# Kernel tuning notes

Hardware: AMD Instinct MI355X
Metric: run time of the kernel (lower is better)

## Reference

```python
import jax, jax.numpy as jnp
import numpy as np

B, C, H, W = 4, 512, 64, 64
C8 = C // 8


def setup_inputs() -> dict:
    key = jax.random.key(0)
    ks = jax.random.split(key, 8)
    return {
        "x": jax.random.normal(ks[0], (B, C, H, W), jnp.float32),
        "wb": jax.random.normal(ks[1], (C8, C), jnp.float32) * 0.05,
        "bb": jax.random.normal(ks[2], (C8,), jnp.float32) * 0.05,
        "wc": jax.random.normal(ks[3], (C8, C), jnp.float32) * 0.05,
        "bc": jax.random.normal(ks[4], (C8,), jnp.float32) * 0.05,
        "wd": jax.random.normal(ks[5], (C, C), jnp.float32) * 0.05,
        "bd": jax.random.normal(ks[6], (C,), jnp.float32) * 0.05,
        "alpha": jax.random.normal(ks[7], (1,), jnp.float32),
    }


def reference(x, wb, bb, wc, bc, wd, bd, alpha):
    b, c, h, w = x.shape
    n = h * w
    xf = x.reshape(b, c, n)  # [B, C, N]
    # 1x1 convs == per-pixel channel matmuls
    feat_b = jnp.einsum('kc,bcn->bkn', wb, xf) + bb[:, None]  # [B, C/8, N]
    feat_c = jnp.einsum('kc,bcn->bkn', wc, xf) + bc[:, None]  # [B, C/8, N]
    # attention_s[n, m] = softmax_m( feat_b[:, n] . feat_c[:, m] )  (no scaling, as in source)
    scores = jnp.einsum('bkn,bkm->bnm', feat_b, feat_c)  # [B, N, N]
    attn = jax.nn.softmax(scores, axis=-1)
    feat_d = jnp.einsum('oc,bcn->bon', wd, xf) + bd[:, None]  # [B, C, N]
    # feat_e = bmm(feat_d, attn^T): fe[c, n] = sum_m fd[c, m] * attn[n, m]
    feat_e = jnp.einsum('bcm,bnm->bcn', feat_d, attn).reshape(b, c, h, w)
    return alpha[0] * feat_e + x
```

## Files before the change

### kernel.cpp

```cpp
#include <hip/hip_runtime.h>
#include <hip/hip_bf16.h>

#define NB 4
#define CC 512
#define CK 64
#define NN 4096

typedef unsigned short u16;
typedef __attribute__((ext_vector_type(8))) __bf16 bf16x8;
typedef __attribute__((ext_vector_type(4))) float f32x4;
typedef __attribute__((ext_vector_type(4))) unsigned int u32x4;
typedef __attribute__((ext_vector_type(8))) unsigned short u16x8;
typedef __attribute__((ext_vector_type(4))) unsigned short u16x4;

__device__ __forceinline__ u16 f2b(float f) {
  union { float f; unsigned u; } x; x.f = f;
  unsigned r = x.u + 0x7fffu + ((x.u >> 16) & 1u);
  return (u16)(r >> 16);
}
__device__ __forceinline__ float b2f(u16 u) {
  union { unsigned u; float f; } x; x.u = ((unsigned)u) << 16; return x.f;
}

#define MFMA16(a, b, c) __builtin_amdgcn_mfma_f32_16x16x32_bf16((a), (b), (c), 0, 0, 0)

__global__ __launch_bounds__(256) void proj_qk(
    const float* __restrict__ x,
    const float* __restrict__ wb, const float* __restrict__ bb,
    const float* __restrict__ wc, const float* __restrict__ bc,
    u16* __restrict__ Qhi, u16* __restrict__ Qlo,
    u16* __restrict__ Khi, u16* __restrict__ Klo)
{
  const int tid = threadIdx.x;
  const int n0 = blockIdx.x * 64;
  const int which = blockIdx.y;
  const int b = blockIdx.z;
  const float* w   = which ? wc : wb;
  const float* bia = which ? bc : bb;
  u16* oh = which ? Khi : Qhi;
  u16* ol = which ? Klo : Qlo;

  __shared__ u16 Wh[64][40], Wl[64][40], Xh[64][40], Xl[64][40];

  const int lane = tid & 63, wid = tid >> 6;
  const int wr = wid >> 1, wn = wid & 1;
  const int l15 = lane & 15, lk = (lane >> 4) * 8;

  f32x4 acc[2][2] = {};

  for (int kk = 0; kk < CC; kk += 32) {
    {
      const int row = tid >> 2, c0 = (tid & 3) * 8;
      const float* src = w + (size_t)row * CC + kk + c0;
#pragma unroll
      for (int i = 0; i < 8; ++i) {
        float v = src[i];
        u16 h = f2b(v);
        Wh[row][c0 + i] = h;
        Wl[row][c0 + i] = f2b(v - b2f(h));
      }
    }
    {
      const int cc2 = tid >> 3, j0 = (tid & 7) * 8;
      const float* src = x + ((size_t)b * CC + kk + cc2) * NN + n0 + j0;
#pragma unroll
      for (int i = 0; i < 8; ++i) {
        float v = src[i];
        u16 h = f2b(v);
        Xh[j0 + i][cc2] = h;
        Xl[j0 + i][cc2] = f2b(v - b2f(h));
      }
    }
    __syncthreads();
#pragma unroll
    for (int fi = 0; fi < 2; ++fi) {
      const int ar = wr * 32 + fi * 16 + l15;
      bf16x8 ah = *(const bf16x8*)&Wh[ar][lk];
      bf16x8 al = *(const bf16x8*)&Wl[ar][lk];
#pragma unroll
      for (int fj = 0; fj < 2; ++fj) {
        const int br = wn * 32 + fj * 16 + l15;
        bf16x8 bh = *(const bf16x8*)&Xh[br][lk];
        bf16x8 bl = *(const bf16x8*)&Xl[br][lk];
        acc[fi][fj] = MFMA16(ah, bh, acc[fi][fj]);
        acc[fi][fj] = MFMA16(ah, bl, acc[fi][fj]);
        acc[fi][fj] = MFMA16(al, bh, acc[fi][fj]);
      }
    }
    __syncthreads();
  }

#pragma unroll
  for (int fi = 0; fi < 2; ++fi) {
    const int d0 = wr * 32 + fi * 16 + (lane >> 4) * 4;
#pragma unroll
    for (int fj = 0; fj < 2; ++fj) {
      const int n = n0 + wn * 32 + fj * 16 + l15;
      u16x4 vh, vl;
#pragma unroll
      for (int r = 0; r < 4; ++r) {
        float v = acc[fi][fj][r] + bia[d0 + r];
        u16 h = f2b(v);
        vh[r] = h;
        vl[r] = f2b(v - b2f(h));
      }
      *(u16x4*)&oh[((size_t)b * NN + n) * CK + d0] = vh;
      *(u16x4*)&ol[((size_t)b * NN + n) * CK + d0] = vl;
    }
  }
}

__global__ __launch_bounds__(256) void proj_v(
    const float* __restrict__ x,
    const float* __restrict__ wd, const float* __restrict__ bd,
    u16* __restrict__ Vt)
{
  const int tid = threadIdx.x;
  const int n0 = blockIdx.x * 64;
  const int o0 = blockIdx.y * 64;
  const int b = blockIdx.z;

  __shared__ u16 Wt[64][40], Xt[64][40];
  const int lane = tid & 63, wid = tid >> 6;
  const int wr = wid >> 1, wn = wid & 1;
  const int l15 = lane & 15, lk = (lane >> 4) * 8;

  f32x4 acc[2][2] = {};
  for (int kk = 0; kk < CC; kk += 32) {
    {
      const int row = tid >> 2, c0 = (tid & 3) * 8;
      const float* src = wd + (size_t)(o0 + row) * CC + kk + c0;
#pragma unroll
      for (int i = 0; i < 8; ++i) Wt[row][c0 + i] = f2b(src[i]);
    }
    {
      const int cc2 = tid >> 3, j0 = (tid & 7) * 8;
      const float* src = x + ((size_t)b * CC + kk + cc2) * NN + n0 + j0;
#pragma unroll
      for (int i = 0; i < 8; ++i) Xt[j0 + i][cc2] = f2b(src[i]);
    }
    __syncthreads();
#pragma unroll
    for (int fi = 0; fi < 2; ++fi) {
      bf16x8 a = *(const bf16x8*)&Wt[wr * 32 + fi * 16 + l15][lk];
#pragma unroll
      for (int fj = 0; fj < 2; ++fj) {
        bf16x8 bv = *(const bf16x8*)&Xt[wn * 32 + fj * 16 + l15][lk];
        acc[fi][fj] = MFMA16(a, bv, acc[fi][fj]);
      }
    }
    __syncthreads();
  }
#pragma unroll
  for (int fi = 0; fi < 2; ++fi) {
    const int d0 = o0 + wr * 32 + fi * 16 + (lane >> 4) * 4;
#pragma unroll
    for (int fj = 0; fj < 2; ++fj) {
      const int n = n0 + wn * 32 + fj * 16 + l15;
#pragma unroll
      for (int r = 0; r < 4; ++r)
        Vt[((size_t)b * CC + d0 + r) * NN + n] = f2b(acc[fi][fj][r] + bd[d0 + r]);
    }
  }
}

struct alignas(16) AttnLds {
  u16 kh[2][64][64];
  u16 kl[2][64][64];
  float s[64][68];
  u16 p[64][64];
  float m[64];
  float l[64];
  float sc[64];
};

__global__ __launch_bounds__(512, 2) void attn(
    const u16* __restrict__ Qhi, const u16* __restrict__ Qlo,
    const u16* __restrict__ Khi, const u16* __restrict__ Klo,
    const u16* __restrict__ Vt,
    const float* __restrict__ x, const float* __restrict__ alpha,
    float* __restrict__ out)
{
  __shared__ AttnLds L;
  const int tid = threadIdx.x;
  const int lane = tid & 63, wid = tid >> 6;
  const int bid = blockIdx.x;
  const int b = (bid & 7) >> 1;
  const int qt = ((bid >> 3) << 1) | (bid & 1);
  const int q0 = qt * 64;
  const int l15 = lane & 15;
  const int lk8 = (lane >> 4) * 8;

  const int fi = wid >> 1;
  const int fj0 = (wid & 1) * 2;

  const int srow = tid >> 3;
  const int sch  = (tid & 7) * 8;
  const int ssw  = sch ^ ((srow & 7) << 3);

  bf16x8 qah[2], qal[2];
  {
    const size_t qg = ((size_t)b * NN + q0 + fi * 16 + l15) * CK + lk8;
    qah[0] = *(const bf16x8*)&Qhi[qg];
    qah[1] = *(const bf16x8*)&Qhi[qg + 32];
    qal[0] = *(const bf16x8*)&Qlo[qg];
    qal[1] = *(const bf16x8*)&Qlo[qg + 32];
  }
  {
    const size_t g = ((size_t)b * NN + srow) * CK + sch;
    u32x4 h  = *(const u32x4*)&Khi[g];
    u32x4 lo = *(const u32x4*)&Klo[g];
    *(u32x4*)&L.kh[0][srow][ssw] = h;
    *(u32x4*)&L.kl[0][srow][ssw] = lo;
  }
  if (tid < 64) { L.m[tid] = -__builtin_huge_valf(); L.l[tid] = 0.f; }

  const u16* vbase = Vt + ((size_t)b * CC + wid * 64 + l15) * NN + lk8;

  f32x4 accO[4][4] = {};

  __syncthreads();

  for (int t = 0; t < 64; ++t) {
    const int m0 = t * 64;
    const int cur = t & 1;
    const bool hasNext = (t < 63);

    u32x4 kh_r, kl_r;
    if (hasNext) {
      const size_t g = ((size_t)b * NN + m0 + 64 + srow) * CK + sch;
      kh_r = *(const u32x4*)&Khi[g];
      kl_r = *(const u32x4*)&Klo[g];
    }
    bf16x8 vr[2][4];
#pragma unroll
    for (int f_ = 0; f_ < 4; ++f_)
#pragma unroll
      for (int ks = 0; ks < 2; ++ks)
        vr[ks][f_] = *(const bf16x8*)(vbase + (size_t)f_ * 16 * NN + m0 + ks * 32);

    __builtin_amdgcn_s_setprio(1);
#pragma unroll
    for (int f2 = 0; f2 < 2; ++f2) {
      const int fj = fj0 + f2;
      f32x4 s = {};
#pragma unroll
      for (int ks = 0; ks < 2; ++ks) {
        const int k = ks * 32 + lk8;
        const int br = fj * 16 + l15;
        bf16x8 bh = *(const bf16x8*)&L.kh[cur][br][k ^ ((br & 7) << 3)];
        bf16x8 bl = *(const bf16x8*)&L.kl[cur][br][k ^ ((br & 7) << 3)];
        s = MFMA16(qah[ks], bh, s);
        s = MFMA16(qah[ks], bl, s);
        s = MFMA16(qal[ks], bh, s);
      }
      const int r0 = fi * 16 + (lane >> 4) * 4, c0 = fj * 16 + l15;
#pragma unroll
      for (int r = 0; r < 4; ++r) L.s[r0 + r][c0] = s[r];
    }
    __builtin_amdgcn_s_setprio(0);
    __syncthreads();

    if (hasNext) {
      *(u32x4*)&L.kh[cur ^ 1][srow][ssw] = kh_r;
      *(u32x4*)&L.kl[cur ^ 1][srow][ssw] = kl_r;
    }
    {
      const int row = srow, sub = tid & 7;
      const float* sr = &L.s[row][sch];
      f32x4 a0 = *(const f32x4*)&sr[0];
      f32x4 a1 = *(const f32x4*)&sr[4];
      float mx = fmaxf(fmaxf(fmaxf(a0[0], a0[1]), fmaxf(a0[2], a0[3])),
                       fmaxf(fmaxf(a1[0], a1[1]), fmaxf(a1[2], a1[3])));
      mx = fmaxf(mx, __shfl_xor(mx, 1));
      mx = fmaxf(mx, __shfl_xor(mx, 2));
      mx = fmaxf(mx, __shfl_xor(mx, 4));
      const float mOld = L.m[row];
      const float mNew = fmaxf(mOld, mx);
      float pv[8], sum = 0.f;
#pragma unroll
      for (int j = 0; j < 4; ++j) { pv[j] = __expf(a0[j] - mNew); sum += pv[j]; }
#pragma unroll
      for (int j = 0; j < 4; ++j) { pv[4 + j] = __expf(a1[j] - mNew); sum += pv[4 + j]; }
      sum += __shfl_xor(sum, 1);
      sum += __shfl_xor(sum, 2);
      sum += __shfl_xor(sum, 4);
      const float scf = __expf(mOld - mNew);
      if (sub == 0) {
        L.m[row] = mNew;
        L.l[row] = L.l[row] * scf + sum;
        L.sc[row] = scf;
      }
      u16x8 pb;
#pragma unroll
      for (int j = 0; j < 8; ++j) pb[j] = f2b(pv[j]);
      *(u16x8*)&L.p[row][ssw] = pb;
    }
    __syncthreads();

#pragma unroll
    for (int f_ = 0; f_ < 4; ++f_) {
      const int r0 = f_ * 16 + (lane >> 4) * 4;
      float s0 = L.sc[r0], s1 = L.sc[r0 + 1], s2 = L.sc[r0 + 2], s3 = L.sc[r0 + 3];
#pragma unroll
      for (int fj = 0; fj < 4; ++fj) {
        accO[f_][fj][0] *= s0; accO[f_][fj][1] *= s1;
        accO[f_][fj][2] *= s2; accO[f_][fj][3] *= s3;
      }
    }
    __builtin_amdgcn_s_setprio(1);
#pragma unroll
    for (int ks = 0; ks < 2; ++ks) {
      const int k = ks * 32 + lk8;
      bf16x8 a[4];
#pragma unroll
      for (int f_ = 0; f_ < 4; ++f_) {
        const int ar = f_ * 16 + l15;
        a[f_] = *(const bf16x8*)&L.p[ar][k ^ ((ar & 7) << 3)];
      }
#pragma unroll
      for (int fj = 0; fj < 4; ++fj)
#pragma unroll
        for (int f_ = 0; f_ < 4; ++f_)
          accO[f_][fj] = MFMA16(a[f_], vr[ks][fj], accO[f_][fj]);
    }
    __builtin_amdgcn_s_setprio(0);
  }
  __syncthreads();
  const float al = alpha[0];
#pragma unroll
  for (int f_ = 0; f_ < 4; ++f_) {
    const int r0 = f_ * 16 + (lane >> 4) * 4;
    const float rl0 = 1.f / L.l[r0],     rl1 = 1.f / L.l[r0 + 1];
    const float rl2 = 1.f / L.l[r0 + 2], rl3 = 1.f / L.l[r0 + 3];
    const int n_ = q0 + r0;
#pragma unroll
    for (int fj = 0; fj < 4; ++fj) {
      const int c_ = wid * 64 + fj * 16 + l15;
      const size_t g = ((size_t)b * CC + c_) * NN + n_;
      f32x4 xv = *(const f32x4*)&x[g];
      f32x4 ov;
      ov[0] = fmaf(al, accO[f_][fj][0] * rl0, xv[0]);
      ov[1] = fmaf(al, accO[f_][fj][1] * rl1, xv[1]);
      ov[2] = fmaf(al, accO[f_][fj][2] * rl2, xv[2]);
      ov[3] = fmaf(al, accO[f_][fj][3] * rl3, xv[3]);
      *(f32x4*)&out[g] = ov;
    }
  }
}

extern "C" void kernel_launch(void* const* d_in, const int* in_sizes, int n_in,
                              void* d_out, int out_size, void* d_ws, size_t ws_size,
                              hipStream_t stream) {
  const float* x     = (const float*)d_in[0];
  const float* wb    = (const float*)d_in[1];
  const float* bb    = (const float*)d_in[2];
  const float* wc    = (const float*)d_in[3];
  const float* bc    = (const float*)d_in[4];
  const float* wd    = (const float*)d_in[5];
  const float* bd    = (const float*)d_in[6];
  const float* alpha = (const float*)d_in[7];
  float* out = (float*)d_out;

  u16* Qhi = (u16*)d_ws;
  u16* Qlo = Qhi + (size_t)NB * NN * CK;
  u16* Khi = Qlo + (size_t)NB * NN * CK;
  u16* Klo = Khi + (size_t)NB * NN * CK;
  u16* Vt  = Klo + (size_t)NB * NN * CK;

  proj_qk<<<dim3(NN / 64, 2, NB), 256, 0, stream>>>(x, wb, bb, wc, bc, Qhi, Qlo, Khi, Klo);
  proj_v<<<dim3(NN / 64, CC / 64, NB), 256, 0, stream>>>(x, wd, bd, Vt);
  attn<<<dim3(256), 512, 0, stream>>>(Qhi, Qlo, Khi, Klo, Vt, x, alpha, out);
}
```

Before: 250.4 us.

## Split attention output channels across two blocks of 256 threads each

The attention kernel now launches 512 blocks of 256 threads instead of 256 blocks of 512. Each block handles one 64-query tile and half of the 512 output channels. Each wave computes a full 16x64 score strip, and the K-tile load and softmax work are redistributed over 4 threads per row. This doubles the block count to fill the CUs better and shrinks per-block size, at the cost of computing QK^T scores and softmax twice per query tile.

After: 233.8 us. 1.07x faster.

```diff
diff --git a/kernel.cpp b/kernel.cpp
--- a/kernel.cpp
+++ b/kernel.cpp
@@ -174,7 +174,7 @@
   float sc[64];
 };
 
-__global__ __launch_bounds__(512, 2) void attn(
+__global__ __launch_bounds__(256, 2) void attn(
     const u16* __restrict__ Qhi, const u16* __restrict__ Qlo,
     const u16* __restrict__ Khi, const u16* __restrict__ Klo,
     const u16* __restrict__ Vt,
@@ -185,22 +185,21 @@
   const int tid = threadIdx.x;
   const int lane = tid & 63, wid = tid >> 6;
   const int bid = blockIdx.x;
-  const int b = (bid & 7) >> 1;
-  const int qt = ((bid >> 3) << 1) | (bid & 1);
+  const int b = (bid >> 1) & 3;
+  const int qt = bid >> 3;
+  const int ohalf = bid & 1;
   const int q0 = qt * 64;
   const int l15 = lane & 15;
   const int lk8 = (lane >> 4) * 8;
 
-  const int fi = wid >> 1;
-  const int fj0 = (wid & 1) * 2;
-
-  const int srow = tid >> 3;
-  const int sch  = (tid & 7) * 8;
-  const int ssw  = sch ^ ((srow & 7) << 3);
+  const int srow = tid >> 2;
+  const int sch  = (tid & 3) * 16;
+  const int ssw0 = sch ^ ((srow & 7) << 3);
+  const int ssw1 = (sch + 8) ^ ((srow & 7) << 3);
 
   bf16x8 qah[2], qal[2];
   {
-    const size_t qg = ((size_t)b * NN + q0 + fi * 16 + l15) * CK + lk8;
+    const size_t qg = ((size_t)b * NN + q0 + wid * 16 + l15) * CK + lk8;
     qah[0] = *(const bf16x8*)&Qhi[qg];
     qah[1] = *(const bf16x8*)&Qhi[qg + 32];
     qal[0] = *(const bf16x8*)&Qlo[qg];
@@ -208,14 +207,14 @@
   }
   {
     const size_t g = ((size_t)b * NN + srow) * CK + sch;
-    u32x4 h  = *(const u32x4*)&Khi[g];
-    u32x4 lo = *(const u32x4*)&Klo[g];
-    *(u32x4*)&L.kh[0][srow][ssw] = h;
-    *(u32x4*)&L.kl[0][srow][ssw] = lo;
+    *(u32x4*)&L.kh[0][srow][ssw0] = *(const u32x4*)&Khi[g];
+    *(u32x4*)&L.kh[0][srow][ssw1] = *(const u32x4*)&Khi[g + 8];
+    *(u32x4*)&L.kl[0][srow][ssw0] = *(const u32x4*)&Klo[g];
+    *(u32x4*)&L.kl[0][srow][ssw1] = *(const u32x4*)&Klo[g + 8];
   }
   if (tid < 64) { L.m[tid] = -__builtin_huge_valf(); L.l[tid] = 0.f; }
 
-  const u16* vbase = Vt + ((size_t)b * CC + wid * 64 + l15) * NN + lk8;
+  const u16* vbase = Vt + ((size_t)b * CC + ohalf * 256 + wid * 64 + l15) * NN + lk8;
 
   f32x4 accO[4][4] = {};
 
@@ -226,11 +225,13 @@
     const int cur = t & 1;
     const bool hasNext = (t < 63);
 
-    u32x4 kh_r, kl_r;
+    u32x4 kh0, kh1, kl0, kl1;
     if (hasNext) {
       const size_t g = ((size_t)b * NN + m0 + 64 + srow) * CK + sch;
-      kh_r = *(const u32x4*)&Khi[g];
-      kl_r = *(const u32x4*)&Klo[g];
+      kh0 = *(const u32x4*)&Khi[g];
+      kh1 = *(const u32x4*)&Khi[g + 8];
+      kl0 = *(const u32x4*)&Klo[g];
+      kl1 = *(const u32x4*)&Klo[g + 8];
     }
     bf16x8 vr[2][4];
 #pragma unroll
@@ -241,8 +242,7 @@
 
     __builtin_amdgcn_s_setprio(1);
 #pragma unroll
-    for (int f2 = 0; f2 < 2; ++f2) {
-      const int fj = fj0 + f2;
+    for (int fj = 0; fj < 4; ++fj) {
       f32x4 s = {};
 #pragma unroll
       for (int ks = 0; ks < 2; ++ks) {
@@ -254,7 +254,7 @@
         s = MFMA16(qah[ks], bl, s);
         s = MFMA16(qal[ks], bh, s);
       }
-      const int r0 = fi * 16 + (lane >> 4) * 4, c0 = fj * 16 + l15;
+      const int r0 = wid * 16 + (lane >> 4) * 4, c0 = fj * 16 + l15;
 #pragma unroll
       for (int r = 0; r < 4; ++r) L.s[r0 + r][c0] = s[r];
     }
@@ -262,39 +262,51 @@
     __syncthreads();
 
     if (hasNext) {
-      *(u32x4*)&L.kh[cur ^ 1][srow][ssw] = kh_r;
-      *(u32x4*)&L.kl[cur ^ 1][srow][ssw] = kl_r;
-    }
-    {
-      const int row = srow, sub = tid & 7;
+      *(u32x4*)&L.kh[cur ^ 1][srow][ssw0] = kh0;
+      *(u32x4*)&L.kh[cur ^ 1][srow][ssw1] = kh1;
+      *(u32x4*)&L.kl[cur ^ 1][srow][ssw0] = kl0;
+      *(u32x4*)&L.kl[cur ^ 1][srow][ssw1] = kl1;
+    }
+    {
+      const int row = srow, sub = tid & 3;
       const float* sr = &L.s[row][sch];
       f32x4 a0 = *(const f32x4*)&sr[0];
       f32x4 a1 = *(const f32x4*)&sr[4];
+      f32x4 a2 = *(const f32x4*)&sr[8];
+      f32x4 a3 = *(const f32x4*)&sr[12];
       float mx = fmaxf(fmaxf(fmaxf(a0[0], a0[1]), fmaxf(a0[2], a0[3])),
                        fmaxf(fmaxf(a1[0], a1[1]), fmaxf(a1[2], a1[3])));
+      mx = fmaxf(mx, fmaxf(fmaxf(fmaxf(a2[0], a2[1]), fmaxf(a2[2], a2[3])),
+                           fmaxf(fmaxf(a3[0], a3[1]), fmaxf(a3[2], a3[3]))));
       mx = fmaxf(mx, __shfl_xor(mx, 1));
       mx = fmaxf(mx, __shfl_xor(mx, 2));
-      mx = fmaxf(mx, __shfl_xor(mx, 4));
       const float mOld = L.m[row];
       const float mNew = fmaxf(mOld, mx);
-      float pv[8], sum = 0.f;
-#pragma unroll
-      for (int j = 0; j < 4; ++j) { pv[j] = __expf(a0[j] - mNew); sum += pv[j]; }
-#pragma unroll
-      for (int j = 0; j < 4; ++j) { pv[4 + j] = __expf(a1[j] - mNew); sum += pv[4 + j]; }
+      float pv[16];
+      float sum = 0.f;
+#pragma unroll
+      for (int j = 0; j < 4; ++j) { pv[j]      = __expf(a0[j] - mNew); sum += pv[j]; }
+#pragma unroll
+      for (int j = 0; j < 4; ++j) { pv[4 + j]  = __expf(a1[j] - mNew); sum += pv[4 + j]; }
+#pragma unroll
+      for (int j = 0; j < 4; ++j) { pv[8 + j]  = __expf(a2[j] - mNew); sum += pv[8 + j]; }
+#pragma unroll
+      for (int j = 0; j < 4; ++j) { pv[12 + j] = __expf(a3[j] - mNew); sum += pv[12 + j]; }
       sum += __shfl_xor(sum, 1);
       sum += __shfl_xor(sum, 2);
-      sum += __shfl_xor(sum, 4);
       const float scf = __expf(mOld - mNew);
       if (sub == 0) {
         L.m[row] = mNew;
         L.l[row] = L.l[row] * scf + sum;
         L.sc[row] = scf;
       }
-      u16x8 pb;
-#pragma unroll
-      for (int j = 0; j < 8; ++j) pb[j] = f2b(pv[j]);
-      *(u16x8*)&L.p[row][ssw] = pb;
+      u16x8 pb0, pb1;
+#pragma unroll
+      for (int j = 0; j < 8; ++j) pb0[j] = f2b(pv[j]);
+#pragma unroll
+      for (int j = 0; j < 8; ++j) pb1[j] = f2b(pv[8 + j]);
+      *(u16x8*)&L.p[row][ssw0] = pb0;
+      *(u16x8*)&L.p[row][ssw1] = pb1;
     }
     __syncthreads();
 
@@ -336,7 +348,7 @@
     const int n_ = q0 + r0;
 #pragma unroll
     for (int fj = 0; fj < 4; ++fj) {
-      const int c_ = wid * 64 + fj * 16 + l15;
+      const int c_ = ohalf * 256 + wid * 64 + fj * 16 + l15;
       const size_t g = ((size_t)b * CC + c_) * NN + n_;
       f32x4 xv = *(const f32x4*)&x[g];
       f32x4 ov;
@@ -370,5 +382,5 @@
 
   proj_qk<<<dim3(NN / 64, 2, NB), 256, 0, stream>>>(x, wb, bb, wc, bc, Qhi, Qlo, Khi, Klo);
   proj_v<<<dim3(NN / 64, CC / 64, NB), 256, 0, stream>>>(x, wd, bd, Vt);
-  attn<<<dim3(256), 512, 0, stream>>>(Qhi, Qlo, Khi, Klo, Vt, x, alpha, out);
-}
+  attn<<<dim3(512), 256, 0, stream>>>(Qhi, Qlo, Khi, Klo, Vt, x, alpha, out);
+}
```
